# Performance work log

Hardware: AMD Instinct MI355X
Metric: run time of the kernel (lower is better)

## Reference

```python
import jax, jax.numpy as jnp
import numpy as np

N = 8192
F_IN = 256
F_OUT = 64
ALPHA = 0.2  # LeakyReLU negative slope
MASK_VAL = -9e15


def setup_inputs() -> dict:
    key = jax.random.key(0)
    k1, k2, k3, k4 = jax.random.split(key, 4)
    h = jax.random.normal(k1, (N, F_IN), dtype=jnp.float32)
    adj = jax.random.randint(k2, (N, N), 0, 2, dtype=jnp.int32)  # 0/1 dense adjacency
    # Parameters (original creates them inside forward with xavier init; here fixed inputs)
    W = jax.random.normal(k3, (F_IN, F_OUT), dtype=jnp.float32) * (1.414 * np.sqrt(2.0 / (F_IN + F_OUT)))
    a = jax.random.normal(k4, (2 * F_OUT, 1), dtype=jnp.float32) * (1.414 * np.sqrt(2.0 / (2 * F_OUT + 1)))
    return {"h": h, "adj": adj, "W": W, "a": a}


def reference(h, adj, W, a):
    # Wh: [N, F_OUT]
    Wh = h @ W
    # e_ij = LeakyReLU(a^T [Wh_i ; Wh_j]) computed via broadcast instead of the
    f_src = Wh @ a[:F_OUT, 0]   # [N] contribution of row node i
    f_dst = Wh @ a[F_OUT:, 0]   # [N] contribution of col node j
    e = jax.nn.leaky_relu(f_src[:, None] + f_dst[None, :], negative_slope=ALPHA)  # [N, N]
    # adj-masked row softmax
    scores = jnp.where(adj > 0, e, MASK_VAL)
    attention = jax.nn.softmax(scores, axis=1)
    # dropout omitted (deterministic eval reference)
    h_prime = attention @ Wh  # [N, F_OUT]
    return jax.nn.elu(h_prime)  # concat=True branch
```

## Files before the change

kernel.cpp:

```cpp
#include <hip/hip_runtime.h>
#include <hip/hip_bf16.h>

#define NN 8192
#define FIN 256
#define FOUT 64
#define L2E 1.4426950408889634f
#define PADK2 72

typedef __attribute__((ext_vector_type(8))) short short8;
typedef __attribute__((ext_vector_type(4))) float f32x4;
typedef __attribute__((ext_vector_type(4))) int   iv4;

#define BAR() do { \
  __asm__ __volatile__("s_waitcnt lgkmcnt(0)" ::: "memory"); \
  __builtin_amdgcn_s_barrier(); \
  __asm__ __volatile__("" ::: "memory"); \
} while (0)

__device__ __forceinline__ unsigned short f2bf(float x){
  unsigned u = __float_as_uint(x);
  u += 0x7FFFu + ((u >> 16) & 1u);
  return (unsigned short)(u >> 16);
}

__device__ __forceinline__ unsigned spread4(unsigned x){
  x &= 0xFFu;
  x = (x | (x << 12)) & 0x000F000Fu;
  x = (x | (x << 6))  & 0x03030303u;
  x = (x | (x << 3))  & 0x11111111u;
  return x;
}

__device__ __forceinline__ void cv_process(iv4 d, int l,
                                           unsigned* __restrict__ mp, int g){
  unsigned n = (unsigned)(d.x != 0)        | ((unsigned)(d.y != 0) << 1)
             | ((unsigned)(d.z != 0) << 2) | ((unsigned)(d.w != 0) << 3);
  unsigned long long B0 = __ballot((n & 1u) != 0);
  unsigned long long B1 = __ballot((n & 2u) != 0);
  unsigned long long B2 = __ballot((n & 4u) != 0);
  unsigned long long B3 = __ballot((n & 8u) != 0);
  const int hi = l & 4, sh = (l & 3) * 8;
  unsigned b0 = (unsigned)((hi ? (B0 >> 32) : B0) >> sh);
  unsigned b1 = (unsigned)((hi ? (B1 >> 32) : B1) >> sh);
  unsigned b2 = (unsigned)((hi ? (B2 >> 32) : B2) >> sh);
  unsigned b3 = (unsigned)((hi ? (B3 >> 32) : B3) >> sh);
  unsigned word = spread4(b0) | (spread4(b1) << 1)
                | (spread4(b2) << 2) | (spread4(b3) << 3);
  if (l < 8) mp[g*8 + l] = word;
}

__global__ __launch_bounds__(256) void k_pm(const float* __restrict__ h,
    const float* __restrict__ W, const float* __restrict__ a,
    const int* __restrict__ adj, unsigned short* __restrict__ WhT,
    float* __restrict__ fs, float* __restrict__ fd,
    unsigned* __restrict__ gmax_u, unsigned* __restrict__ mask){
  const int bid = blockIdx.x, t = threadIdx.x;
  const int l = t & 63, wv = t >> 6;
  if (bid % 3 == 0){
    const int pid = bid / 3;
    __shared__ float Ws[128*64];
    __shared__ float hs[8][128];
    const int rb = pid * 8;
    float acc0 = 0.f, acc1 = 0.f;
    for (int half = 0; half < 2; ++half){
      if (half) __syncthreads();
      for (int i = t; i < 2048; i += 256)
        ((float4*)Ws)[i] = ((const float4*)W)[half*2048 + i];
      {
        int rr = t >> 5, cc = t & 31;
        ((float4*)&hs[rr][0])[cc] =
            *(const float4*)(h + (size_t)(rb+rr)*FIN + half*128 + cc*4);
      }
      __syncthreads();
      #pragma unroll 8
      for (int k = 0; k < 128; ++k){
        float wval = Ws[k*64 + l];
        acc0 = fmaf(hs[wv*2+0][k], wval, acc0);
        acc1 = fmaf(hs[wv*2+1][k], wval, acc1);
      }
    }
    const int r0 = rb + wv*2, r1 = r0 + 1;
    float a1 = a[l], a2 = a[64 + l];
    float p0 = acc0*a1, q0 = acc0*a2, p1 = acc1*a1, q1 = acc1*a2;
    #pragma unroll
    for (int m = 1; m < 64; m <<= 1){
      p0 += __shfl_xor(p0, m); q0 += __shfl_xor(q0, m);
      p1 += __shfl_xor(p1, m); q1 += __shfl_xor(q1, m);
    }
    if (l == 0){
      fs[r0] = p0*L2E; fs[r1] = p1*L2E; fd[r0] = q0*L2E; fd[r1] = q1*L2E;
      atomicMax(gmax_u, __float_as_uint(q0*L2E + 64.0f));
      atomicMax(gmax_u, __float_as_uint(q1*L2E + 64.0f));
    }
    WhT[(size_t)l*NN + r0] = f2bf(acc0);
    WhT[(size_t)l*NN + r1] = f2bf(acc1);
  } else {
    const int cid = bid - bid/3 - 1;
    const unsigned rowid = (unsigned)cid*4u + (unsigned)wv;
    const iv4* __restrict__ ap = (const iv4*)(adj + (size_t)rowid*8192u) + l;
    unsigned* __restrict__ mp = mask + rowid*256u;
    iv4 d0 = ap[0*64], d1 = ap[1*64], d2 = ap[2*64], d3 = ap[3*64];
    iv4 d4 = ap[4*64], d5 = ap[5*64], d6 = ap[6*64], d7 = ap[7*64];
    #pragma unroll 1
    for (int i = 0; i < 32; i += 8){
      cv_process(d0, l, mp, i+0); if (i+ 8 < 32) d0 = ap[(i+ 8)*64];
      cv_process(d1, l, mp, i+1); if (i+ 9 < 32) d1 = ap[(i+ 9)*64];
      cv_process(d2, l, mp, i+2); if (i+10 < 32) d2 = ap[(i+10)*64];
      cv_process(d3, l, mp, i+3); if (i+11 < 32) d3 = ap[(i+11)*64];
      cv_process(d4, l, mp, i+4); if (i+12 < 32) d4 = ap[(i+12)*64];
      cv_process(d5, l, mp, i+5); if (i+13 < 32) d5 = ap[(i+13)*64];
      cv_process(d6, l, mp, i+6); if (i+14 < 32) d6 = ap[(i+14)*64];
      cv_process(d7, l, mp, i+7); if (i+15 < 32) d7 = ap[(i+15)*64];
    }
  }
}

__device__ __forceinline__ void attn_math(unsigned mbits, f32x4 fv0, f32x4 fv1,
    short8 w0, short8 w1, short8 w2, short8 w3,
    float fsrL, float mL, f32x4* acc, float& s0, float& s1){
  const float fv[8] = {fv0[0],fv0[1],fv0[2],fv0[3], fv1[0],fv1[1],fv1[2],fv1[3]};
  float w[8];
  #pragma unroll
  for (int j = 0; j < 8; ++j){
    float x  = fsrL + fv[j];
    float tt = fmaxf(x, 0.2f*x);
    float e  = __builtin_amdgcn_exp2f(tt - mL);
    w[j] = (mbits & (1u << j)) ? e : 0.0f;
  }
  s0 += (w[0]+w[2]) + (w[4]+w[6]);
  s1 += (w[1]+w[3]) + (w[5]+w[7]);
  short8 af;
  __hip_bfloat162* afp = (__hip_bfloat162*)&af;
  #pragma unroll
  for (int j = 0; j < 4; ++j)
    afp[j] = __float22bfloat162_rn(make_float2(w[2*j], w[2*j+1]));
  acc[0] = __builtin_amdgcn_mfma_f32_16x16x32_bf16(af, w0, acc[0], 0,0,0);
  acc[1] = __builtin_amdgcn_mfma_f32_16x16x32_bf16(af, w1, acc[1], 0,0,0);
  acc[2] = __builtin_amdgcn_mfma_f32_16x16x32_bf16(af, w2, acc[2], 0,0,0);
  acc[3] = __builtin_amdgcn_mfma_f32_16x16x32_bf16(af, w3, acc[3], 0,0,0);
}

__global__ __launch_bounds__(256, 4) void k_attn(const unsigned* __restrict__ mask,
    const unsigned short* __restrict__ WhT, const float* __restrict__ fs,
    const float* __restrict__ fd, const unsigned* __restrict__ gmax_u,
    float* __restrict__ acc_out, float* __restrict__ s_out){
  __shared__ unsigned short bslab[2][64*PADK2];
  __shared__ float fslab[2][64];
  const int t = threadIdx.x, l = t & 63, wv = t >> 6;
  const int g = blockIdx.x & 127;
  const int kchunk = blockIdx.x >> 7;
  const int row = l & 15, quad = l >> 4;
  const int ibase = g*64 + wv*16;
  const int irow  = ibase + row;
  const float gmaxL = __uint_as_float(*gmax_u) - 64.0f;
  const float fsrL  = fs[irow];
  const float xL    = fsrL + gmaxL;
  const float mL    = fmaxf(xL, 0.2f*xL);

  const unsigned jbase = (unsigned)kchunk*1024u;
  const unsigned m_off = (unsigned)irow*256u + (jbase >> 5);
  const unsigned sg_off = (unsigned)l*8192u + jbase + (unsigned)wv*16u;
  const int      sl_off = l*PADK2 + wv*16;
  const int      qsh    = quad*8;

  f32x4 acc[4];
  #pragma unroll
  for (int nb = 0; nb < 4; ++nb) acc[nb] = (f32x4){0.f,0.f,0.f,0.f};

  {
    short8 v0 = *(const short8*)(WhT + sg_off);
    short8 v1 = *(const short8*)(WhT + sg_off + 8);
    *(short8*)&bslab[0][sl_off]     = v0;
    *(short8*)&bslab[0][sl_off + 8] = v1;
    if (t < 64) fslab[0][t] = fd[jbase + t];
  }
  unsigned m0a = mask[m_off + 0] >> qsh, m0b = mask[m_off + 1] >> qsh;
  unsigned m1a = mask[m_off + 2] >> qsh, m1b = mask[m_off + 3] >> qsh;

  float s0 = 0.f, s1 = 0.f;
  short8 nw0, nw1; float nf = 0.f;

  #pragma unroll 1
  for (int s = 0; s < 16; s += 2){
    BAR();
    nw0 = *(const short8*)(WhT + sg_off + (s+1)*64);
    nw1 = *(const short8*)(WhT + sg_off + (s+1)*64 + 8);
    if (t < 64) nf = fd[jbase + (s+1)*64 + t];
    {
      f32x4 fv0 = *(const f32x4*)&fslab[0][qsh];
      f32x4 fv1 = *(const f32x4*)&fslab[0][qsh + 4];
      short8 w0 = *(const short8*)&bslab[0][( 0 + row)*PADK2 + qsh];
      short8 w1 = *(const short8*)&bslab[0][(16 + row)*PADK2 + qsh];
      short8 w2 = *(const short8*)&bslab[0][(32 + row)*PADK2 + qsh];
      short8 w3 = *(const short8*)&bslab[0][(48 + row)*PADK2 + qsh];
      attn_math(m0a, fv0, fv1, w0, w1, w2, w3, fsrL, mL, acc, s0, s1);
      fv0 = *(const f32x4*)&fslab[0][32 + qsh];
      fv1 = *(const f32x4*)&fslab[0][32 + qsh + 4];
      w0 = *(const short8*)&bslab[0][( 0 + row)*PADK2 + 32 + qsh];
      w1 = *(const short8*)&bslab[0][(16 + row)*PADK2 + 32 + qsh];
      w2 = *(const short8*)&bslab[0][(32 + row)*PADK2 + 32 + qsh];
      w3 = *(const short8*)&bslab[0][(48 + row)*PADK2 + 32 + qsh];
      attn_math(m0b, fv0, fv1, w0, w1, w2, w3, fsrL, mL, acc, s0, s1);
    }
    if (s + 2 < 16){
      m0a = mask[m_off + (s+2)*2]     >> qsh;
      m0b = mask[m_off + (s+2)*2 + 1] >> qsh;
    }
    *(short8*)&bslab[1][sl_off]     = nw0;
    *(short8*)&bslab[1][sl_off + 8] = nw1;
    if (t < 64) fslab[1][t] = nf;

    BAR();
    if (s + 2 < 16){
      nw0 = *(const short8*)(WhT + sg_off + (s+2)*64);
      nw1 = *(const short8*)(WhT + sg_off + (s+2)*64 + 8);
      if (t < 64) nf = fd[jbase + (s+2)*64 + t];
    }
    {
      f32x4 fv0 = *(const f32x4*)&fslab[1][qsh];
      f32x4 fv1 = *(const f32x4*)&fslab[1][qsh + 4];
      short8 w0 = *(const short8*)&bslab[1][( 0 + row)*PADK2 + qsh];
      short8 w1 = *(const short8*)&bslab[1][(16 + row)*PADK2 + qsh];
      short8 w2 = *(const short8*)&bslab[1][(32 + row)*PADK2 + qsh];
      short8 w3 = *(const short8*)&bslab[1][(48 + row)*PADK2 + qsh];
      attn_math(m1a, fv0, fv1, w0, w1, w2, w3, fsrL, mL, acc, s0, s1);
      fv0 = *(const f32x4*)&fslab[1][32 + qsh];
      fv1 = *(const f32x4*)&fslab[1][32 + qsh + 4];
      w0 = *(const short8*)&bslab[1][( 0 + row)*PADK2 + 32 + qsh];
      w1 = *(const short8*)&bslab[1][(16 + row)*PADK2 + 32 + qsh];
      w2 = *(const short8*)&bslab[1][(32 + row)*PADK2 + 32 + qsh];
      w3 = *(const short8*)&bslab[1][(48 + row)*PADK2 + 32 + qsh];
      attn_math(m1b, fv0, fv1, w0, w1, w2, w3, fsrL, mL, acc, s0, s1);
    }
    if (s + 3 < 16){
      m1a = mask[m_off + (s+3)*2]     >> qsh;
      m1b = mask[m_off + (s+3)*2 + 1] >> qsh;
    }
    if (s + 2 < 16){
      *(short8*)&bslab[0][sl_off]     = nw0;
      *(short8*)&bslab[0][sl_off + 8] = nw1;
      if (t < 64) fslab[0][t] = nf;
    }
  }

  float sacc = s0 + s1;
  sacc += __shfl_xor(sacc, 16);
  sacc += __shfl_xor(sacc, 32);
  if (l < 16) s_out[kchunk*NN + ibase + l] = sacc;
  float* op = acc_out + ((size_t)kchunk*NN + ibase)*FOUT;
  #pragma unroll
  for (int nb = 0; nb < 4; ++nb)
    #pragma unroll
    for (int r = 0; r < 4; ++r)
      op[(quad*4 + r)*FOUT + nb*16 + row] = acc[nb][r];
}

__global__ __launch_bounds__(256) void k_out(const float* __restrict__ acc,
    const float* __restrict__ s, float* __restrict__ out){
  const int idx = blockIdx.x*256 + threadIdx.x;
  const int i = idx >> 6;
  float num = 0.f, den = 0.f;
  #pragma unroll
  for (int ks = 0; ks < 8; ++ks){
    num += acc[idx + (size_t)ks*(NN*FOUT)];
    den += s[i + ks*NN];
  }
  float x = num / den;
  out[idx] = (x > 0.f) ? x : (__expf(x) - 1.0f);
}

extern "C" void kernel_launch(void* const* d_in, const int* in_sizes, int n_in,
                              void* d_out, int out_size, void* d_ws, size_t ws_size,
                              hipStream_t stream){
  const float* h   = (const float*)d_in[0];
  const int*   adj = (const int*)d_in[1];
  const float* W   = (const float*)d_in[2];
  const float* a   = (const float*)d_in[3];
  char* ws = (char*)d_ws;
  unsigned short* WhT = (unsigned short*)ws;
  float*    fs     = (float*)(ws + (1u<<20));
  float*    fd     = (float*)(ws + (1u<<20) + 32768);
  unsigned* gmax_u = (unsigned*)(ws + (1u<<20) + 65536);
  float*    acc    = (float*)(ws + (2u<<20));
  float*    s_ws   = (float*)(ws + (20u<<20));
  unsigned* mask   = (unsigned*)(ws + (48u<<20));

  (void)hipMemsetAsync(gmax_u, 0, 4, stream);
  k_pm<<<3072, 256, 0, stream>>>(h, W, a, adj, WhT, fs, fd, gmax_u, mask);
  k_attn<<<1024, 256, 0, stream>>>(mask, WhT, fs, fd, gmax_u, acc, s_ws);
  k_out<<<2048, 256, 0, stream>>>(acc, s_ws, (float*)d_out);
}
```

Measured before the change: 432.9 us.

## Widen attention blocks to 128 rows sharing staged Wh tile; vectorize output kernel

The attention kernel now runs 512-thread blocks covering 128 query rows, so each staged 64x64 Wh^T slab in LDS is reused by 8 wavefronts instead of 4. That halves the global Wh loads per row and splits the staging work so each thread copies one short8 instead of two. The output reduction kernel now processes float4 per thread and multiplies by a reciprocal instead of dividing. The larger blocks may reduce occupancy flexibility and make barrier waits longer.

```diff
diff --git a/kernel.cpp b/kernel.cpp
--- a/kernel.cpp
+++ b/kernel.cpp
@@ -140,17 +140,17 @@
   acc[3] = __builtin_amdgcn_mfma_f32_16x16x32_bf16(af, w3, acc[3], 0,0,0);
 }
 
-__global__ __launch_bounds__(256, 4) void k_attn(const unsigned* __restrict__ mask,
+__global__ __launch_bounds__(512, 4) void k_attn(const unsigned* __restrict__ mask,
     const unsigned short* __restrict__ WhT, const float* __restrict__ fs,
     const float* __restrict__ fd, const unsigned* __restrict__ gmax_u,
     float* __restrict__ acc_out, float* __restrict__ s_out){
   __shared__ unsigned short bslab[2][64*PADK2];
   __shared__ float fslab[2][64];
   const int t = threadIdx.x, l = t & 63, wv = t >> 6;
-  const int g = blockIdx.x & 127;
-  const int kchunk = blockIdx.x >> 7;
+  const int g = blockIdx.x & 63;
+  const int kchunk = blockIdx.x >> 6;
   const int row = l & 15, quad = l >> 4;
-  const int ibase = g*64 + wv*16;
+  const int ibase = g*128 + wv*16;
   const int irow  = ibase + row;
   const float gmaxL = __uint_as_float(*gmax_u) - 64.0f;
   const float fsrL  = fs[irow];
@@ -159,8 +159,8 @@
 
   const unsigned jbase = (unsigned)kchunk*1024u;
   const unsigned m_off = (unsigned)irow*256u + (jbase >> 5);
-  const unsigned sg_off = (unsigned)l*8192u + jbase + (unsigned)wv*16u;
-  const int      sl_off = l*PADK2 + wv*16;
+  const unsigned sg_off = (unsigned)(t & 63)*8192u + jbase + (unsigned)wv*8u;
+  const int      sl_off = (t & 63)*PADK2 + wv*8;
   const int      qsh    = quad*8;
 
   f32x4 acc[4];
@@ -168,23 +168,19 @@
   for (int nb = 0; nb < 4; ++nb) acc[nb] = (f32x4){0.f,0.f,0.f,0.f};
 
   {
-    short8 v0 = *(const short8*)(WhT + sg_off);
-    short8 v1 = *(const short8*)(WhT + sg_off + 8);
-    *(short8*)&bslab[0][sl_off]     = v0;
-    *(short8*)&bslab[0][sl_off + 8] = v1;
+    *(short8*)&bslab[0][sl_off] = *(const short8*)(WhT + sg_off);
     if (t < 64) fslab[0][t] = fd[jbase + t];
   }
   unsigned m0a = mask[m_off + 0] >> qsh, m0b = mask[m_off + 1] >> qsh;
   unsigned m1a = mask[m_off + 2] >> qsh, m1b = mask[m_off + 3] >> qsh;
 
   float s0 = 0.f, s1 = 0.f;
-  short8 nw0, nw1; float nf = 0.f;
+  short8 nw; float nf = 0.f;
 
   #pragma unroll 1
   for (int s = 0; s < 16; s += 2){
     BAR();
-    nw0 = *(const short8*)(WhT + sg_off + (s+1)*64);
-    nw1 = *(const short8*)(WhT + sg_off + (s+1)*64 + 8);
+    nw = *(const short8*)(WhT + sg_off + (s+1)*64);
     if (t < 64) nf = fd[jbase + (s+1)*64 + t];
     {
       f32x4 fv0 = *(const f32x4*)&fslab[0][qsh];
@@ -206,14 +202,12 @@
       m0a = mask[m_off + (s+2)*2]     >> qsh;
       m0b = mask[m_off + (s+2)*2 + 1] >> qsh;
     }
-    *(short8*)&bslab[1][sl_off]     = nw0;
-    *(short8*)&bslab[1][sl_off + 8] = nw1;
+    *(short8*)&bslab[1][sl_off] = nw;
     if (t < 64) fslab[1][t] = nf;
 
     BAR();
     if (s + 2 < 16){
-      nw0 = *(const short8*)(WhT + sg_off + (s+2)*64);
-      nw1 = *(const short8*)(WhT + sg_off + (s+2)*64 + 8);
+      nw = *(const short8*)(WhT + sg_off + (s+2)*64);
       if (t < 64) nf = fd[jbase + (s+2)*64 + t];
     }
     {
@@ -237,8 +231,7 @@
       m1b = mask[m_off + (s+3)*2 + 1] >> qsh;
     }
     if (s + 2 < 16){
-      *(short8*)&bslab[0][sl_off]     = nw0;
-      *(short8*)&bslab[0][sl_off + 8] = nw1;
+      *(short8*)&bslab[0][sl_off] = nw;
       if (t < 64) fslab[0][t] = nf;
     }
   }
@@ -257,16 +250,24 @@
 
 __global__ __launch_bounds__(256) void k_out(const float* __restrict__ acc,
     const float* __restrict__ s, float* __restrict__ out){
-  const int idx = blockIdx.x*256 + threadIdx.x;
-  const int i = idx >> 6;
-  float num = 0.f, den = 0.f;
+  const int idx4 = blockIdx.x*256 + threadIdx.x;
+  const int i = idx4 >> 4;
+  float4 num = make_float4(0.f,0.f,0.f,0.f);
+  float den = 0.f;
   #pragma unroll
   for (int ks = 0; ks < 8; ++ks){
-    num += acc[idx + (size_t)ks*(NN*FOUT)];
+    float4 v = ((const float4*)acc)[idx4 + ks*(NN*FOUT/4)];
+    num.x += v.x; num.y += v.y; num.z += v.z; num.w += v.w;
     den += s[i + ks*NN];
   }
-  float x = num / den;
-  out[idx] = (x > 0.f) ? x : (__expf(x) - 1.0f);
+  const float rd = 1.0f / den;
+  float4 o;
+  float x;
+  x = num.x*rd; o.x = (x > 0.f) ? x : (__expf(x) - 1.0f);
+  x = num.y*rd; o.y = (x > 0.f) ? x : (__expf(x) - 1.0f);
+  x = num.z*rd; o.z = (x > 0.f) ? x : (__expf(x) - 1.0f);
+  x = num.w*rd; o.w = (x > 0.f) ? x : (__expf(x) - 1.0f);
+  ((float4*)out)[idx4] = o;
 }
 
 extern "C" void kernel_launch(void* const* d_in, const int* in_sizes, int n_in,
@@ -287,6 +288,6 @@
 
   (void)hipMemsetAsync(gmax_u, 0, 4, stream);
   k_pm<<<3072, 256, 0, stream>>>(h, W, a, adj, WhT, fs, fd, gmax_u, mask);
-  k_attn<<<1024, 256, 0, stream>>>(mask, WhT, fs, fd, gmax_u, acc, s_ws);
-  k_out<<<2048, 256, 0, stream>>>(acc, s_ws, (float*)d_out);
-}
+  k_attn<<<512, 512, 0, stream>>>(mask, WhT, fs, fd, gmax_u, acc, s_ws);
+  k_out<<<512, 256, 0, stream>>>(acc, s_ws, (float*)d_out);
+}
```

New measurement: 433.7 us. About the same (+0.2%).
